# Performance work log

Hardware: AMD Instinct MI355X
Metric: run time of the kernel (lower is better)

Reference implementation:

```python
import jax, jax.numpy as jnp
from jax import lax
import numpy as np

D_MODEL = 2048
NUM_EXPERTS = 16
NUM_TOKENS = 8192  # must be divisible by NUM_EXPERTS (balanced assignment)


def setup_inputs() -> dict:
    key = jax.random.key(0)
    k1, k2 = jax.random.split(key)
    features = jax.random.normal(k1, (NUM_TOKENS, D_MODEL), dtype=jnp.float32)
    # gate weight (orthogonal init in torch; gaussian is fine for a numerical baseline)
    W = jax.random.normal(k2, (NUM_EXPERTS, D_MODEL), dtype=jnp.float32) * 0.1
    b = jnp.zeros((NUM_EXPERTS,), dtype=jnp.float32)
    return {"features": features, "W": W, "b": b, "is_training": 1}


def _balanced_assignment(scores):
    """Greedy balanced assignment: each expert receives exactly T//E tokens.
    Deterministic stand-in for the cpp auction-based balanced_assignment: scan
    over tokens, each token takes its best-scoring expert with remaining capacity.
    Returns sort_by_expert: token indices sorted (stably) by assigned expert."""
    T, E = scores.shape
    cap_per_expert = T // E

    def step(cap, s):  # cap: [E] remaining capacity, s: [E] token's scores
        masked = jnp.where(cap > 0, s, -jnp.inf)
        e = jnp.argmax(masked)
        return cap.at[e].add(-1), e

    _, tok2exp = lax.scan(step, jnp.full((E,), cap_per_expert, dtype=jnp.int32), scores)
    sort_by_expert = jnp.argsort(tok2exp, stable=True)  # [T] token ids grouped by expert
    return sort_by_expert


def reference(features, W, b, is_training):
    # gating computed under no_grad in the original
    affinities = lax.stop_gradient(features @ W.T + b)  # [T, E]
    T, E = affinities.shape
    cap = T // E

    sort_by_expert = _balanced_assignment(affinities)

    routing_probs = jax.nn.softmax(affinities, axis=1)  # [T, E]

    # gather_scores: permute probs into expert order, pick each token's score for
    # its assigned expert, then un-permute back to original token order.
    sorted_probs = routing_probs[sort_by_expert]                 # [T, E]
    expert_idx = (jnp.arange(T) // cap)[:, None]                 # [T, 1], balanced splits
    gathered = jnp.take_along_axis(sorted_probs, expert_idx, axis=1)  # [T, 1]
    i_sort = jnp.argsort(sort_by_expert)                         # inverse permutation
    gathered_scores = gathered[i_sort]                           # [T, 1]

    return sort_by_expert, gathered_scores
```

## Files before the change

### kernel.cpp

```cpp
#include <hip/hip_runtime.h>
#include <hip/hip_bf16.h>
#include <math.h>

#define T_TOK 8192
#define D_MODEL 2048
#define N_EXP 16
#define CAP 512
#define NSEG (T_TOK / 64)


__device__ __forceinline__ unsigned int f2ord(float f) {
    unsigned int b = __float_as_uint(f);
    return (b & 0x80000000u) ? ~b : (b | 0x80000000u);
}

__global__ __launch_bounds__(256, 4) void gemm_aff_kernel(
    const float* __restrict__ feat, const float* __restrict__ W,
    float* __restrict__ aff)
{
    const int tid  = threadIdx.x;
    const int wave = tid >> 6, lane = tid & 63;
    const int tbase = blockIdx.x * 16 + wave * 4;

    const float* fbase = feat + (size_t)tbase * D_MODEL + lane * 4;

    float acc[64];
    #pragma unroll
    for (int i = 0; i < 64; ++i) acc[i] = 0.f;

    float4 cur[4], nxt[4];
    #pragma unroll
    for (int r = 0; r < 4; ++r)
        cur[r] = *(const float4*)(fbase + (size_t)r * D_MODEL);

    #pragma unroll
    for (int j = 0; j < 8; ++j) {
        if (j < 7) {
            #pragma unroll
            for (int r = 0; r < 4; ++r)
                nxt[r] = *(const float4*)(fbase + (size_t)r * D_MODEL + (j + 1) * 256);
        }
        const float* wbase = W + j * 256 + lane * 4;
        #pragma unroll
        for (int g = 0; g < 4; ++g) {
            float4 wv[4];
            #pragma unroll
            for (int i = 0; i < 4; ++i)
                wv[i] = *(const float4*)(wbase + (size_t)(g * 4 + i) * D_MODEL);
            #pragma unroll
            for (int i = 0; i < 4; ++i)
                #pragma unroll
                for (int r = 0; r < 4; ++r) {
                    acc[r * 16 + g * 4 + i] += cur[r].x * wv[i].x;
                    acc[r * 16 + g * 4 + i] += cur[r].y * wv[i].y;
                    acc[r * 16 + g * 4 + i] += cur[r].z * wv[i].z;
                    acc[r * 16 + g * 4 + i] += cur[r].w * wv[i].w;
                }
        }
        #pragma unroll
        for (int r = 0; r < 4; ++r) cur[r] = nxt[r];
    }

    #pragma unroll
    for (int step = 0; step < 6; ++step) {
        const int m    = 1 << step;
        const int half = 64 >> (step + 1);
        const bool hi  = (lane & m) != 0;
        #pragma unroll
        for (int jj = 0; jj < half; ++jj) {
            float send = hi ? acc[jj] : acc[jj + half];
            float recv = __shfl_xor(send, m, 64);
            acc[jj] = (hi ? acc[jj + half] : acc[jj]) + recv;
        }
    }
    const int slot = ((lane & 1) << 5) | (((lane >> 1) & 1) << 4) | (((lane >> 2) & 1) << 3)
                   | (((lane >> 3) & 1) << 2) | (((lane >> 4) & 1) << 1) | ((lane >> 5) & 1);
    const int r = slot >> 4, e = slot & 15;
    aff[(size_t)(tbase + r) * N_EXP + e] = acc[0];
}

__global__ __launch_bounds__(256) void finalize_kernel(
    const float* __restrict__ aff_in, const float* __restrict__ bias,
    unsigned long long* __restrict__ pref, float* __restrict__ probs)
{
    const int t = blockIdx.x * 256 + threadIdx.x;

    float aff[N_EXP];
    const float4* p = (const float4*)(aff_in + (size_t)t * N_EXP);
    #pragma unroll
    for (int q = 0; q < 4; ++q) {
        float4 v = p[q];
        aff[q*4+0] = v.x; aff[q*4+1] = v.y; aff[q*4+2] = v.z; aff[q*4+3] = v.w;
    }
    #pragma unroll
    for (int e = 0; e < N_EXP; ++e) aff[e] += bias[e];

    float m = aff[0];
    #pragma unroll
    for (int e = 1; e < N_EXP; ++e) m = fmaxf(m, aff[e]);
    float s = 0.f;
    #pragma unroll
    for (int e = 0; e < N_EXP; ++e) s += __expf(aff[e] - m);

    float4* pr = (float4*)(probs + (size_t)t * N_EXP);
    #pragma unroll
    for (int q = 0; q < 4; ++q) {
        float4 v;
        v.x = __expf(aff[q*4+0] - m) / s;
        v.y = __expf(aff[q*4+1] - m) / s;
        v.z = __expf(aff[q*4+2] - m) / s;
        v.w = __expf(aff[q*4+3] - m) / s;
        pr[q] = v;
    }

    unsigned long long key[N_EXP];
    #pragma unroll
    for (int j = 0; j < N_EXP; ++j)
        key[j] = ((unsigned long long)f2ord(aff[j]) << 4) | (unsigned long long)(15 - j);
    unsigned long long pk = 0ull;
    unsigned int used = 0;
    for (int r = 0; r < N_EXP; ++r) {
        unsigned long long bk = 0ull; int be = 0;
        for (int j = 0; j < N_EXP; ++j)
            if (!((used >> j) & 1u) && key[j] > bk) { bk = key[j]; be = j; }
        used |= (1u << be);
        pk = (pk << 4) | (unsigned long long)be;
    }
    pref[t] = pk;
}

__global__ __launch_bounds__(512) void events_kernel(
    const unsigned long long* __restrict__ pref, int* __restrict__ evt)
{
    __shared__ unsigned long long prefL[T_TOK];
    __shared__ unsigned long long segmask[N_EXP][NSEG + 1];
    __shared__ int pseg[N_EXP][NSEG + 1];
    __shared__ int rem_cap[N_EXP], fparr[N_EXP];
    __shared__ int s_avail, s_pmin, s_fe, s_seglo;
    __shared__ int evp[N_EXP], evf[N_EXP];

    const int tid  = threadIdx.x;
    const int wave = tid >> 6, lane = tid & 63;
    const unsigned long long lt_mask = (1ull << lane) - 1ull;

    for (int i = tid; i < T_TOK; i += 512) prefL[i] = pref[i];
    if (tid < N_EXP) rem_cap[tid] = CAP;
    if (tid == 0) { s_avail = 0xFFFF; s_seglo = 0; }
    __syncthreads();

    for (int s = wave; s < NSEG; s += 8) {
        int c = (int)(prefL[s * 64 + lane] >> 60);
        #pragma unroll
        for (int e = 0; e < N_EXP; ++e) {
            unsigned long long mm = __ballot(c == e);
            if (lane == e) segmask[e][s] = mm;
        }
    }
    __syncthreads();

    for (int round = 0; round < N_EXP; ++round) {
        const unsigned int avail = (unsigned int)s_avail;

        #pragma unroll
        for (int ee = 0; ee < 2; ++ee) {
            const int e = wave + ee * 8;
            const unsigned long long m0 = segmask[e][lane];
            const unsigned long long m1 = segmask[e][64 + lane];
            const int c0 = (int)__popcll(m0), c1 = (int)__popcll(m1);
            int v0 = c0;
            #pragma unroll
            for (int d = 1; d < 64; d <<= 1) {
                int o = __shfl_up(v0, d, 64);
                if (lane >= d) v0 += o;
            }
            const int excl0 = v0 - c0;
            const int tot0  = __shfl(v0, 63, 64);
            int v1 = c1;
            #pragma unroll
            for (int d = 1; d < 64; d <<= 1) {
                int o = __shfl_up(v1, d, 64);
                if (lane >= d) v1 += o;
            }
            const int excl1 = tot0 + v1 - c1;
            pseg[e][lane]      = excl0;
            pseg[e][64 + lane] = excl1;

            int fp = 0x7FFFFFFF;
            if ((avail >> e) & 1u) {
                const int need = rem_cap[e];
                int segc = -1, kk = 0;
                if (excl0 < need && excl0 + c0 >= need)      { segc = lane;      kk = need - excl0; }
                else if (excl1 < need && excl1 + c1 >= need) { segc = 64 + lane; kk = need - excl1; }
                unsigned long long b = __ballot(segc >= 0);
                if (b) {
                    int l2    = __builtin_ctzll(b);
                    int sstar = __shfl(segc, l2, 64);
                    int k2    = __shfl(kk,   l2, 64);
                    unsigned long long m = segmask[e][sstar];
                    int rr = (int)__popcll(m & lt_mask);
                    bool hit = ((m >> lane) & 1ull) && (rr == k2 - 1);
                    unsigned long long hb = __ballot(hit);
                    fp = sstar * 64 + __builtin_ctzll(hb);
                }
            }
            if (lane == 0) fparr[e] = fp;
        }
        __syncthreads();

        if (tid == 0) {
            int pm = 0x7FFFFFFF, f = 0;
            #pragma unroll
            for (int e = 0; e < N_EXP; ++e)
                if (fparr[e] < pm) { pm = fparr[e]; f = e; }
            s_pmin = pm; s_fe = f;
        }
        __syncthreads();
        const int pmin = s_pmin, fe = s_fe;
        const int segF = pmin >> 6;
        const int seglo = s_seglo;

        if (tid < N_EXP) {
            const int e = tid;
            unsigned long long mlep = ((pmin & 63) == 63) ? ~0ull
                                      : ((1ull << ((pmin & 63) + 1)) - 1ull);
            unsigned long long m = segmask[e][segF];
            rem_cap[e] -= pseg[e][segF] + (int)__popcll(m & mlep);
            segmask[e][segF] = m & ~mlep;
        }
        for (int i = tid; i < (segF - seglo) * N_EXP; i += 512)
            segmask[i & 15][seglo + (i >> 4)] = 0ull;
        if (tid == 0) {
            evp[round] = pmin; evf[round] = fe;
            s_avail = (int)(avail & ~(1u << fe));
            s_seglo = segF;
        }
        __syncthreads();

        if (round < N_EXP - 1) {
            const unsigned int navail = avail & ~(1u << fe);
            for (int s = segF + wave; s < NSEG; s += 8) {
                unsigned long long m = segmask[fe][s];
                if (m) {
                    if ((m >> lane) & 1ull) {
                        unsigned long long pp = prefL[s * 64 + lane];
                        int e2 = (int)(pp >> 60);
                        while (!((navail >> e2) & 1u)) { pp <<= 4; e2 = (int)(pp >> 60); }
                        atomicOr(&segmask[e2][s], 1ull << lane);
                    }
                    if (lane == 0) segmask[fe][s] = 0ull;
                }
            }
        }
        __syncthreads();
    }

    if (tid < N_EXP) { evt[tid] = evp[tid]; evt[N_EXP + tid] = evf[tid]; }
}

__global__ __launch_bounds__(256) void choice_kernel(
    const unsigned long long* __restrict__ pref, const int* __restrict__ evt,
    unsigned char* __restrict__ t2e, int* __restrict__ bcnt)
{
    __shared__ int evp[N_EXP], evf[N_EXP];
    __shared__ int sc[4][N_EXP];
    const int tid = threadIdx.x, b = blockIdx.x;
    const int wave = tid >> 6, lane = tid & 63;
    if (tid < N_EXP) evp[tid] = evt[tid];
    else if (tid < 2 * N_EXP) evf[tid - N_EXP] = evt[tid];
    __syncthreads();

    const int t = b * 256 + tid;
    unsigned int mask = 0xFFFFu;
    #pragma unroll
    for (int j = 0; j < N_EXP; ++j)
        if (evp[j] < t) mask &= ~(1u << evf[j]);

    unsigned long long pp = pref[t];
    int e = (int)(pp >> 60);
    while (!((mask >> e) & 1u)) { pp <<= 4; e = (int)(pp >> 60); }
    t2e[t] = (unsigned char)e;

    #pragma unroll
    for (int e2 = 0; e2 < N_EXP; ++e2) {
        unsigned long long mm = __ballot(e == e2);
        if (lane == e2) sc[wave][e2] = (int)__popcll(mm);
    }
    __syncthreads();
    if (tid < N_EXP)
        bcnt[b * N_EXP + tid] = sc[0][tid] + sc[1][tid] + sc[2][tid] + sc[3][tid];
}

__global__ __launch_bounds__(256) void writeout_kernel(
    const unsigned char* __restrict__ t2e, const int* __restrict__ bcnt,
    const float* __restrict__ probs,
    float* __restrict__ out0, float* __restrict__ out1)
{
    __shared__ int base[N_EXP];
    __shared__ int sc[4][N_EXP];
    const int tid = threadIdx.x, b = blockIdx.x;
    const int wave = tid >> 6, lane = tid & 63;
    const unsigned long long lt_mask = (1ull << lane) - 1ull;

    const int t = b * 256 + tid;
    const int c = (int)t2e[t];

    unsigned long long own = 0ull;
    #pragma unroll
    for (int e2 = 0; e2 < N_EXP; ++e2) {
        unsigned long long mm = __ballot(c == e2);
        if (c == e2) own = mm;
        if (lane == e2) sc[wave][e2] = (int)__popcll(mm);
    }
    if (tid < N_EXP) {
        int s = 0;
        for (int b2 = 0; b2 < b; ++b2) s += bcnt[b2 * N_EXP + tid];
        base[tid] = s;
    }
    __syncthreads();

    int rank = (int)__popcll(own & lt_mask);
    for (int w2 = 0; w2 < wave; ++w2) rank += sc[w2][c];
    const int pos = base[c] + rank;
    out0[c * CAP + pos] = (float)t;
    out1[t] = probs[(size_t)t * N_EXP + c];
}

extern "C" void kernel_launch(void* const* d_in, const int* in_sizes, int n_in,
                              void* d_out, int out_size, void* d_ws, size_t ws_size,
                              hipStream_t stream) {
    const float* feat = (const float*)d_in[0];
    const float* W    = (const float*)d_in[1];
    const float* bias = (const float*)d_in[2];

    float* out = (float*)d_out;
    char*  ws  = (char*)d_ws;

    float* aff               = (float*)ws;
    unsigned long long* pref = (unsigned long long*)(ws + 524288);
    float* probs             = (float*)(ws + 589824);
    int* evt                 = (int*)(ws + 1114112);
    unsigned char* t2e       = (unsigned char*)(ws + 1114240);
    int* bcnt                = (int*)(ws + 1122432);

    hipLaunchKernelGGL(gemm_aff_kernel, dim3(512), dim3(256), 0, stream,
                       feat, W, aff);
    hipLaunchKernelGGL(finalize_kernel, dim3(T_TOK / 256), dim3(256), 0, stream,
                       aff, bias, pref, probs);
    hipLaunchKernelGGL(events_kernel, dim3(1), dim3(512), 0, stream,
                       pref, evt);
    hipLaunchKernelGGL(choice_kernel, dim3(T_TOK / 256), dim3(256), 0, stream,
                       pref, evt, t2e, bcnt);
    hipLaunchKernelGGL(writeout_kernel, dim3(T_TOK / 256), dim3(256), 0, stream,
                       t2e, bcnt, probs, out, out + T_TOK);
}
```

Measured before the change: 193.9 us.

## Stage gate weights in double-buffered LDS and halve tokens per wave

```diff
diff --git a/kernel.cpp b/kernel.cpp
--- a/kernel.cpp
+++ b/kernel.cpp
@@ -18,53 +18,77 @@
     const float* __restrict__ feat, const float* __restrict__ W,
     float* __restrict__ aff)
 {
+    __shared__ float wlds[2][N_EXP][256];
+
     const int tid  = threadIdx.x;
     const int wave = tid >> 6, lane = tid & 63;
-    const int tbase = blockIdx.x * 16 + wave * 4;
+    const int tbase = blockIdx.x * 8 + wave * 2;
 
     const float* fbase = feat + (size_t)tbase * D_MODEL + lane * 4;
-
-    float acc[64];
-    #pragma unroll
-    for (int i = 0; i < 64; ++i) acc[i] = 0.f;
-
-    float4 cur[4], nxt[4];
-    #pragma unroll
-    for (int r = 0; r < 4; ++r)
+    const float* wsrc0 = W + (size_t)(wave * 4) * D_MODEL + lane * 4;
+
+    float acc[32];
+    #pragma unroll
+    for (int i = 0; i < 32; ++i) acc[i] = 0.f;
+
+    float4 wstage[4];
+    #pragma unroll
+    for (int i = 0; i < 4; ++i)
+        wstage[i] = *(const float4*)(wsrc0 + (size_t)i * D_MODEL);
+
+    float4 cur[2], nxt[2];
+    #pragma unroll
+    for (int r = 0; r < 2; ++r)
         cur[r] = *(const float4*)(fbase + (size_t)r * D_MODEL);
+
+    #pragma unroll
+    for (int i = 0; i < 4; ++i)
+        *(float4*)(&wlds[0][wave * 4 + i][0] + lane * 4) = wstage[i];
+    __syncthreads();
 
     #pragma unroll
     for (int j = 0; j < 8; ++j) {
         if (j < 7) {
             #pragma unroll
-            for (int r = 0; r < 4; ++r)
+            for (int i = 0; i < 4; ++i)
+                wstage[i] = *(const float4*)(wsrc0 + (size_t)i * D_MODEL + (j + 1) * 256);
+            #pragma unroll
+            for (int r = 0; r < 2; ++r)
                 nxt[r] = *(const float4*)(fbase + (size_t)r * D_MODEL + (j + 1) * 256);
         }
-        const float* wbase = W + j * 256 + lane * 4;
+
+        const float* wl = &wlds[j & 1][0][0] + lane * 4;
         #pragma unroll
         for (int g = 0; g < 4; ++g) {
             float4 wv[4];
             #pragma unroll
             for (int i = 0; i < 4; ++i)
-                wv[i] = *(const float4*)(wbase + (size_t)(g * 4 + i) * D_MODEL);
+                wv[i] = *(const float4*)(wl + (g * 4 + i) * 256);
             #pragma unroll
             for (int i = 0; i < 4; ++i)
                 #pragma unroll
-                for (int r = 0; r < 4; ++r) {
+                for (int r = 0; r < 2; ++r) {
                     acc[r * 16 + g * 4 + i] += cur[r].x * wv[i].x;
                     acc[r * 16 + g * 4 + i] += cur[r].y * wv[i].y;
                     acc[r * 16 + g * 4 + i] += cur[r].z * wv[i].z;
                     acc[r * 16 + g * 4 + i] += cur[r].w * wv[i].w;
                 }
         }
-        #pragma unroll
-        for (int r = 0; r < 4; ++r) cur[r] = nxt[r];
-    }
-
-    #pragma unroll
-    for (int step = 0; step < 6; ++step) {
+
+        if (j < 7) {
+            #pragma unroll
+            for (int i = 0; i < 4; ++i)
+                *(float4*)(&wlds[(j + 1) & 1][wave * 4 + i][0] + lane * 4) = wstage[i];
+            #pragma unroll
+            for (int r = 0; r < 2; ++r) cur[r] = nxt[r];
+        }
+        __syncthreads();
+    }
+
+    #pragma unroll
+    for (int step = 0; step < 5; ++step) {
         const int m    = 1 << step;
-        const int half = 64 >> (step + 1);
+        const int half = 16 >> step;
         const bool hi  = (lane & m) != 0;
         #pragma unroll
         for (int jj = 0; jj < half; ++jj) {
@@ -73,10 +97,14 @@
             acc[jj] = (hi ? acc[jj + half] : acc[jj]) + recv;
         }
     }
-    const int slot = ((lane & 1) << 5) | (((lane >> 1) & 1) << 4) | (((lane >> 2) & 1) << 3)
-                   | (((lane >> 3) & 1) << 2) | (((lane >> 4) & 1) << 1) | ((lane >> 5) & 1);
-    const int r = slot >> 4, e = slot & 15;
-    aff[(size_t)(tbase + r) * N_EXP + e] = acc[0];
+    acc[0] += __shfl_xor(acc[0], 32, 64);
+
+    if (lane < 32) {
+        const int slot = ((lane & 1) << 4) | (((lane >> 1) & 1) << 3) | (((lane >> 2) & 1) << 2)
+                       | (((lane >> 3) & 1) << 1) | ((lane >> 4) & 1);
+        const int r = slot >> 4, e = slot & 15;
+        aff[(size_t)(tbase + r) * N_EXP + e] = acc[0];
+    }
 }
 
 __global__ __launch_bounds__(256) void finalize_kernel(
@@ -342,7 +370,7 @@
     unsigned char* t2e       = (unsigned char*)(ws + 1114240);
     int* bcnt                = (int*)(ws + 1122432);
 
-    hipLaunchKernelGGL(gemm_aff_kernel, dim3(512), dim3(256), 0, stream,
+    hipLaunchKernelGGL(gemm_aff_kernel, dim3(1024), dim3(256), 0, stream,
                        feat, W, aff);
     hipLaunchKernelGGL(finalize_kernel, dim3(T_TOK / 256), dim3(256), 0, stream,
                        aff, bias, pref, probs);
```

Measured after the change: 312.4 us. +61.1%, slower.

## Stage feature tile in LDS and split experts across waves in gating GEMM

Applied to the files above, without the earlier changes.

```diff
diff --git a/kernel.cpp b/kernel.cpp
--- a/kernel.cpp
+++ b/kernel.cpp
@@ -14,57 +14,64 @@
     return (b & 0x80000000u) ? ~b : (b | 0x80000000u);
 }
 
-__global__ __launch_bounds__(256, 4) void gemm_aff_kernel(
+__global__ __launch_bounds__(512, 4) void gemm_aff_kernel(
     const float* __restrict__ feat, const float* __restrict__ W,
     float* __restrict__ aff)
 {
+    __shared__ float flds[8][D_MODEL];
+
     const int tid  = threadIdx.x;
     const int wave = tid >> 6, lane = tid & 63;
-    const int tbase = blockIdx.x * 16 + wave * 4;
-
-    const float* fbase = feat + (size_t)tbase * D_MODEL + lane * 4;
-
-    float acc[64];
-    #pragma unroll
-    for (int i = 0; i < 64; ++i) acc[i] = 0.f;
-
-    float4 cur[4], nxt[4];
-    #pragma unroll
-    for (int r = 0; r < 4; ++r)
-        cur[r] = *(const float4*)(fbase + (size_t)r * D_MODEL);
+    const int tbase = blockIdx.x * 8;
+
+    {
+        const float4* src = (const float4*)(feat + (size_t)tbase * D_MODEL);
+        float4* dst = (float4*)&flds[0][0];
+        #pragma unroll
+        for (int i = 0; i < 8; ++i)
+            dst[tid + i * 512] = src[tid + i * 512];
+    }
+
+    const float* w0 = W + (size_t)(wave * 2) * D_MODEL + lane * 4;
+    const float* w1 = w0 + D_MODEL;
+
+    float acc[16];
+    #pragma unroll
+    for (int i = 0; i < 16; ++i) acc[i] = 0.f;
+
+    float4 wv0 = *(const float4*)(w0);
+    float4 wv1 = *(const float4*)(w1);
+    __syncthreads();
 
     #pragma unroll
     for (int j = 0; j < 8; ++j) {
+        float4 wn0, wn1;
         if (j < 7) {
-            #pragma unroll
-            for (int r = 0; r < 4; ++r)
-                nxt[r] = *(const float4*)(fbase + (size_t)r * D_MODEL + (j + 1) * 256);
-        }
-        const float* wbase = W + j * 256 + lane * 4;
-        #pragma unroll
-        for (int g = 0; g < 4; ++g) {
-            float4 wv[4];
-            #pragma unroll
-            for (int i = 0; i < 4; ++i)
-                wv[i] = *(const float4*)(wbase + (size_t)(g * 4 + i) * D_MODEL);
-            #pragma unroll
-            for (int i = 0; i < 4; ++i)
-                #pragma unroll
-                for (int r = 0; r < 4; ++r) {
-                    acc[r * 16 + g * 4 + i] += cur[r].x * wv[i].x;
-                    acc[r * 16 + g * 4 + i] += cur[r].y * wv[i].y;
-                    acc[r * 16 + g * 4 + i] += cur[r].z * wv[i].z;
-                    acc[r * 16 + g * 4 + i] += cur[r].w * wv[i].w;
-                }
-        }
-        #pragma unroll
-        for (int r = 0; r < 4; ++r) cur[r] = nxt[r];
-    }
-
-    #pragma unroll
-    for (int step = 0; step < 6; ++step) {
+            wn0 = *(const float4*)(w0 + (j + 1) * 256);
+            wn1 = *(const float4*)(w1 + (j + 1) * 256);
+        } else {
+            wn0 = wv0; wn1 = wv1;
+        }
+        const float* fl = &flds[0][0] + j * 256 + lane * 4;
+        #pragma unroll
+        for (int r = 0; r < 8; ++r) {
+            float4 f = *(const float4*)(fl + r * D_MODEL);
+            acc[r * 2 + 0] += f.x * wv0.x;
+            acc[r * 2 + 0] += f.y * wv0.y;
+            acc[r * 2 + 0] += f.z * wv0.z;
+            acc[r * 2 + 0] += f.w * wv0.w;
+            acc[r * 2 + 1] += f.x * wv1.x;
+            acc[r * 2 + 1] += f.y * wv1.y;
+            acc[r * 2 + 1] += f.z * wv1.z;
+            acc[r * 2 + 1] += f.w * wv1.w;
+        }
+        wv0 = wn0; wv1 = wn1;
+    }
+
+    #pragma unroll
+    for (int step = 0; step < 4; ++step) {
         const int m    = 1 << step;
-        const int half = 64 >> (step + 1);
+        const int half = 8 >> step;
         const bool hi  = (lane & m) != 0;
         #pragma unroll
         for (int jj = 0; jj < half; ++jj) {
@@ -73,10 +80,15 @@
             acc[jj] = (hi ? acc[jj + half] : acc[jj]) + recv;
         }
     }
-    const int slot = ((lane & 1) << 5) | (((lane >> 1) & 1) << 4) | (((lane >> 2) & 1) << 3)
-                   | (((lane >> 3) & 1) << 2) | (((lane >> 4) & 1) << 1) | ((lane >> 5) & 1);
-    const int r = slot >> 4, e = slot & 15;
-    aff[(size_t)(tbase + r) * N_EXP + e] = acc[0];
+    acc[0] += __shfl_xor(acc[0], 16, 64);
+    acc[0] += __shfl_xor(acc[0], 32, 64);
+
+    if (lane < 16) {
+        const int slot = ((lane & 1) << 3) | (((lane >> 1) & 1) << 2)
+                       | (((lane >> 2) & 1) << 1) | ((lane >> 3) & 1);
+        const int r = slot >> 1, el = slot & 1;
+        aff[(size_t)(tbase + r) * N_EXP + wave * 2 + el] = acc[0];
+    }
 }
 
 __global__ __launch_bounds__(256) void finalize_kernel(
@@ -342,7 +354,7 @@
     unsigned char* t2e       = (unsigned char*)(ws + 1114240);
     int* bcnt                = (int*)(ws + 1122432);
 
-    hipLaunchKernelGGL(gemm_aff_kernel, dim3(512), dim3(256), 0, stream,
+    hipLaunchKernelGGL(gemm_aff_kernel, dim3(T_TOK / 8), dim3(512), 0, stream,
                        feat, W, aff);
     hipLaunchKernelGGL(finalize_kernel, dim3(T_TOK / 256), dim3(256), 0, stream,
                        aff, bias, pref, probs);
```

Result: faster. 187.7 us (-3.2%).
